# Optimization experiments

Hardware: AMD Instinct MI355X
Metric: run time of the kernel (lower is better)

The kernel has to match this reference:

```python
import jax, jax.numpy as jnp
import numpy as np
from jax.scipy.special import digamma, gammaln

COEF = 0.01
PRIOR = 1.0
IGNORE_INDEX = 255


def setup_inputs() -> dict:
    key = jax.random.key(0)
    k1, k2 = jax.random.split(key)
    pred = jax.random.normal(k1, (8, 19, 512, 512), dtype=jnp.float32)
    target = jax.random.randint(k2, (8, 512, 512), 0, 19, dtype=jnp.int64)
    return {"pred": pred, "target": target}


def reference(pred, target):
    # pred: [B, C, H, W] logits; target: [B, H, W] int class ids
    alphas = jnp.exp(pred)
    mask_ignore = target == IGNORE_INDEX
    tgt = jnp.where(mask_ignore, 0, target)
    # gather alpha at the answer class: [B, H, W]
    a_ans = jnp.take_along_axis(alphas, tgt[:, None, :, :], axis=1)[:, 0]
    a_zero = jnp.sum(alphas, axis=1)  # [B, H, W]
    ll_loss = digamma(a_ans) - digamma(a_zero)
    loss1 = gammaln(a_zero) - jnp.sum(gammaln(alphas), axis=1)
    loss2 = jnp.sum((alphas - PRIOR) * (digamma(alphas) - digamma(a_zero)[:, None, :, :]), axis=1)
    kl_loss = loss1 + loss2
    loss = COEF * kl_loss - ll_loss  # [B, H, W]
    loss = jnp.where(mask_ignore, jnp.zeros_like(loss), loss)
    avg_factor = jnp.sum(target != IGNORE_INDEX).astype(loss.dtype)
    return jnp.sum(loss) / avg_factor
```

## Files before the change

kernel.cpp:

```cpp
#include <hip/hip_runtime.h>


#define NCLS 19
#define HW (512 * 512)
#define NPIX (8 * HW)
#define IGNORE_IDX 255

#define PC1 0.08333333333f
#define PC2 0.00833333333f
#define PC3 0.00396825397f
#define GL1 0.08333333333f
#define GL2 0.00277777778f
#define GL3 0.00079365079f
#define HLN2PI 0.9189385332f
#define SUM_HLN2PI 17.45983213f

__device__ __forceinline__ float fast_rcp(float x) { return __builtin_amdgcn_rcpf(x); }

struct Acc {
    float a0, s2, slgy, sx, dgans;
};

__device__ __forceinline__ void chan(float x, int c, int tc, Acc& A) {
    float a   = __expf(x);
    float y   = a + 1.f;
    float rpy = fast_rcp(a * y);
    float r   = a * rpy;
    float rp  = y * rpy;
    float ly  = __logf(y);
    float r2  = r * r;
    float T   = __fmaf_rn(-r2, __fmaf_rn(-r2, PC3, PC2), PC1);
    float psiy = __fmaf_rn(-r2, T, __fmaf_rn(-0.5f, r, ly));
    float psia = psiy - rp;
    A.s2 = __fmaf_rn(a - 1.f, psia, A.s2);
    A.a0 += a;
    float G   = __fmaf_rn(-r2, __fmaf_rn(-r2, GL3, GL2), GL1);
    float lgp = __fmaf_rn(y - 0.5f, ly, -y);
    A.slgy = __fmaf_rn(r, G, A.slgy + lgp);
    A.sx += x;
    A.dgans = (c == tc) ? psia : A.dgans;
}

__device__ __forceinline__ float finish(const Acc& A) {
    float a0  = A.a0;
    float y   = a0 + 1.f;
    float rpy = fast_rcp(a0 * y);
    float r   = a0 * rpy;
    float rp  = y * rpy;
    float ly  = __logf(y);
    float la  = __logf(a0);
    float r2  = r * r;
    float T   = __fmaf_rn(-r2, __fmaf_rn(-r2, PC3, PC2), PC1);
    float psi0 = __fmaf_rn(-r2, T, __fmaf_rn(-0.5f, r, ly)) - rp;
    float G   = __fmaf_rn(-r2, __fmaf_rn(-r2, GL3, GL2), GL1);
    float lg0 = __fmaf_rn(y - 0.5f, ly, -y) + HLN2PI + r * G - la;

    float sum_lg = A.slgy + SUM_HLN2PI - A.sx;
    float ll    = A.dgans - psi0;
    float loss1 = lg0 - sum_lg;
    float loss2 = A.s2 - psi0 * (a0 - (float)NCLS);
    return 0.01f * (loss1 + loss2) - ll;
}

__global__ __launch_bounds__(256, 2) void bml_main(const float* __restrict__ pred,
                                                   const int* __restrict__ target,
                                                   double* __restrict__ ws) {
    int tid = blockIdx.x * blockDim.x + threadIdx.x;
    int p4  = tid << 2;
    int b   = p4 >> 18;
    int hw  = p4 & (HW - 1);
    const float4* base = (const float4*)(pred + (size_t)b * NCLS * HW + hw);

    int4 t4 = *(const int4*)(target + p4);
    int tc0 = (t4.x == IGNORE_IDX) ? 0 : t4.x;
    int tc1 = (t4.y == IGNORE_IDX) ? 0 : t4.y;
    int tc2 = (t4.z == IGNORE_IDX) ? 0 : t4.z;
    int tc3 = (t4.w == IGNORE_IDX) ? 0 : t4.w;

    float4 xs[NCLS];
    #pragma unroll
    for (int c = 0; c < NCLS; ++c)
        xs[c] = base[c * (HW / 4)];
    __builtin_amdgcn_sched_barrier(0);

    Acc A0 = {0.f, 0.f, 0.f, 0.f, 0.f};
    Acc A1 = {0.f, 0.f, 0.f, 0.f, 0.f};
    Acc A2 = {0.f, 0.f, 0.f, 0.f, 0.f};
    Acc A3 = {0.f, 0.f, 0.f, 0.f, 0.f};
    #pragma unroll
    for (int c = 0; c < NCLS; ++c) {
        chan(xs[c].x, c, tc0, A0);
        chan(xs[c].y, c, tc1, A1);
        chan(xs[c].z, c, tc2, A2);
        chan(xs[c].w, c, tc3, A3);
    }

    float l0 = finish(A0), l1 = finish(A1), l2 = finish(A2), l3 = finish(A3);

    float local = 0.f;
    unsigned cnt = 0;
    if (t4.x != IGNORE_IDX) { local += l0; cnt++; }
    if (t4.y != IGNORE_IDX) { local += l1; cnt++; }
    if (t4.z != IGNORE_IDX) { local += l2; cnt++; }
    if (t4.w != IGNORE_IDX) { local += l3; cnt++; }

    #pragma unroll
    for (int off = 32; off; off >>= 1) {
        local += __shfl_down(local, off);
        cnt   += __shfl_down(cnt, off);
    }
    __shared__ float s_sum[4];
    __shared__ unsigned s_cnt[4];
    int lane = threadIdx.x & 63, wid = threadIdx.x >> 6;
    if (lane == 0) { s_sum[wid] = local; s_cnt[wid] = cnt; }
    __syncthreads();
    if (threadIdx.x == 0) {
        float bs = s_sum[0] + s_sum[1] + s_sum[2] + s_sum[3];
        unsigned bc = s_cnt[0] + s_cnt[1] + s_cnt[2] + s_cnt[3];
        atomicAdd(&ws[0], (double)bs);
        atomicAdd(&ws[1], (double)bc);
    }
}

__global__ void bml_finalize(const double* __restrict__ ws, float* __restrict__ out) {
    if (threadIdx.x == 0 && blockIdx.x == 0)
        out[0] = (float)(ws[0] / ws[1]);
}

extern "C" void kernel_launch(void* const* d_in, const int* in_sizes, int n_in,
                              void* d_out, int out_size, void* d_ws, size_t ws_size,
                              hipStream_t stream) {
    const float* pred = (const float*)d_in[0];
    const int* target = (const int*)d_in[1];
    float* out = (float*)d_out;
    double* ws = (double*)d_ws;

    hipMemsetAsync(d_ws, 0, 2 * sizeof(double), stream);

    const int block = 256;
    const int grid = NPIX / (block * 4);
    bml_main<<<grid, block, 0, stream>>>(pred, target, ws);
    bml_finalize<<<1, 64, 0, stream>>>(ws, out);
}
```

Measured before the change: 244.3 us.

## Replace double atomics and memset with per-block partials and tree-reduced finalize

Each block now writes its partial sum and count to its own slot in the workspace, and a 256-thread finalize kernel reduces those slots in double precision. This removes the memset launch and the 4096 contended double atomicAdds. The change also folds the sum-of-x accumulator into the lgamma accumulator, moves the target load after the pred loads, and raises launch_bounds occupancy from 2 to 4 blocks per CU, which may force register spilling given 76 live float values per thread.

```diff
diff --git a/kernel.cpp b/kernel.cpp
--- a/kernel.cpp
+++ b/kernel.cpp
@@ -4,6 +4,7 @@
 #define NCLS 19
 #define HW (512 * 512)
 #define NPIX (8 * HW)
+#define NBLK 2048
 #define IGNORE_IDX 255
 
 #define PC1 0.08333333333f
@@ -18,7 +19,7 @@
 __device__ __forceinline__ float fast_rcp(float x) { return __builtin_amdgcn_rcpf(x); }
 
 struct Acc {
-    float a0, s2, slgy, sx, dgans;
+    float a0, s2, slgx, dgans;
 };
 
 __device__ __forceinline__ void chan(float x, int c, int tc, Acc& A) {
@@ -35,9 +36,8 @@
     A.s2 = __fmaf_rn(a - 1.f, psia, A.s2);
     A.a0 += a;
     float G   = __fmaf_rn(-r2, __fmaf_rn(-r2, GL3, GL2), GL1);
-    float lgp = __fmaf_rn(y - 0.5f, ly, -y);
-    A.slgy = __fmaf_rn(r, G, A.slgy + lgp);
-    A.sx += x;
+    float lgp = __fmaf_rn(y - 0.5f, ly, -y) - x;
+    A.slgx = __fmaf_rn(r, G, A.slgx + lgp);
     A.dgans = (c == tc) ? psia : A.dgans;
 }
 
@@ -55,38 +55,38 @@
     float G   = __fmaf_rn(-r2, __fmaf_rn(-r2, GL3, GL2), GL1);
     float lg0 = __fmaf_rn(y - 0.5f, ly, -y) + HLN2PI + r * G - la;
 
-    float sum_lg = A.slgy + SUM_HLN2PI - A.sx;
+    float sum_lg = A.slgx + SUM_HLN2PI;
     float ll    = A.dgans - psi0;
     float loss1 = lg0 - sum_lg;
     float loss2 = A.s2 - psi0 * (a0 - (float)NCLS);
     return 0.01f * (loss1 + loss2) - ll;
 }
 
-__global__ __launch_bounds__(256, 2) void bml_main(const float* __restrict__ pred,
+__global__ __launch_bounds__(256, 4) void bml_main(const float* __restrict__ pred,
                                                    const int* __restrict__ target,
-                                                   double* __restrict__ ws) {
+                                                   float* __restrict__ partial) {
     int tid = blockIdx.x * blockDim.x + threadIdx.x;
     int p4  = tid << 2;
     int b   = p4 >> 18;
     int hw  = p4 & (HW - 1);
     const float4* base = (const float4*)(pred + (size_t)b * NCLS * HW + hw);
 
+    float4 xs[NCLS];
+    #pragma unroll
+    for (int c = 0; c < NCLS; ++c)
+        xs[c] = base[c * (HW / 4)];
     int4 t4 = *(const int4*)(target + p4);
+    __builtin_amdgcn_sched_barrier(0);
+
     int tc0 = (t4.x == IGNORE_IDX) ? 0 : t4.x;
     int tc1 = (t4.y == IGNORE_IDX) ? 0 : t4.y;
     int tc2 = (t4.z == IGNORE_IDX) ? 0 : t4.z;
     int tc3 = (t4.w == IGNORE_IDX) ? 0 : t4.w;
 
-    float4 xs[NCLS];
-    #pragma unroll
-    for (int c = 0; c < NCLS; ++c)
-        xs[c] = base[c * (HW / 4)];
-    __builtin_amdgcn_sched_barrier(0);
-
-    Acc A0 = {0.f, 0.f, 0.f, 0.f, 0.f};
-    Acc A1 = {0.f, 0.f, 0.f, 0.f, 0.f};
-    Acc A2 = {0.f, 0.f, 0.f, 0.f, 0.f};
-    Acc A3 = {0.f, 0.f, 0.f, 0.f, 0.f};
+    Acc A0 = {0.f, 0.f, 0.f, 0.f};
+    Acc A1 = {0.f, 0.f, 0.f, 0.f};
+    Acc A2 = {0.f, 0.f, 0.f, 0.f};
+    Acc A3 = {0.f, 0.f, 0.f, 0.f};
     #pragma unroll
     for (int c = 0; c < NCLS; ++c) {
         chan(xs[c].x, c, tc0, A0);
@@ -98,11 +98,11 @@
     float l0 = finish(A0), l1 = finish(A1), l2 = finish(A2), l3 = finish(A3);
 
     float local = 0.f;
-    unsigned cnt = 0;
-    if (t4.x != IGNORE_IDX) { local += l0; cnt++; }
-    if (t4.y != IGNORE_IDX) { local += l1; cnt++; }
-    if (t4.z != IGNORE_IDX) { local += l2; cnt++; }
-    if (t4.w != IGNORE_IDX) { local += l3; cnt++; }
+    float cnt = 0.f;
+    if (t4.x != IGNORE_IDX) { local += l0; cnt += 1.f; }
+    if (t4.y != IGNORE_IDX) { local += l1; cnt += 1.f; }
+    if (t4.z != IGNORE_IDX) { local += l2; cnt += 1.f; }
+    if (t4.w != IGNORE_IDX) { local += l3; cnt += 1.f; }
 
     #pragma unroll
     for (int off = 32; off; off >>= 1) {
@@ -110,21 +110,37 @@
         cnt   += __shfl_down(cnt, off);
     }
     __shared__ float s_sum[4];
-    __shared__ unsigned s_cnt[4];
+    __shared__ float s_cnt[4];
     int lane = threadIdx.x & 63, wid = threadIdx.x >> 6;
     if (lane == 0) { s_sum[wid] = local; s_cnt[wid] = cnt; }
     __syncthreads();
     if (threadIdx.x == 0) {
-        float bs = s_sum[0] + s_sum[1] + s_sum[2] + s_sum[3];
-        unsigned bc = s_cnt[0] + s_cnt[1] + s_cnt[2] + s_cnt[3];
-        atomicAdd(&ws[0], (double)bs);
-        atomicAdd(&ws[1], (double)bc);
+        partial[blockIdx.x]        = s_sum[0] + s_sum[1] + s_sum[2] + s_sum[3];
+        partial[NBLK + blockIdx.x] = s_cnt[0] + s_cnt[1] + s_cnt[2] + s_cnt[3];
     }
 }
 
-__global__ void bml_finalize(const double* __restrict__ ws, float* __restrict__ out) {
-    if (threadIdx.x == 0 && blockIdx.x == 0)
-        out[0] = (float)(ws[0] / ws[1]);
+__global__ __launch_bounds__(256) void bml_finalize(const float* __restrict__ partial,
+                                                    float* __restrict__ out) {
+    double s = 0.0, n = 0.0;
+    for (int i = threadIdx.x; i < NBLK; i += 256) {
+        s += (double)partial[i];
+        n += (double)partial[NBLK + i];
+    }
+    #pragma unroll
+    for (int off = 32; off; off >>= 1) {
+        s += __shfl_down(s, off);
+        n += __shfl_down(n, off);
+    }
+    __shared__ double sh_s[4], sh_n[4];
+    int lane = threadIdx.x & 63, wid = threadIdx.x >> 6;
+    if (lane == 0) { sh_s[wid] = s; sh_n[wid] = n; }
+    __syncthreads();
+    if (threadIdx.x == 0) {
+        double ts = sh_s[0] + sh_s[1] + sh_s[2] + sh_s[3];
+        double tn = sh_n[0] + sh_n[1] + sh_n[2] + sh_n[3];
+        out[0] = (float)(ts / tn);
+    }
 }
 
 extern "C" void kernel_launch(void* const* d_in, const int* in_sizes, int n_in,
@@ -133,12 +149,9 @@
     const float* pred = (const float*)d_in[0];
     const int* target = (const int*)d_in[1];
     float* out = (float*)d_out;
-    double* ws = (double*)d_ws;
-
-    hipMemsetAsync(d_ws, 0, 2 * sizeof(double), stream);
+    float* partial = (float*)d_ws;
 
     const int block = 256;
-    const int grid = NPIX / (block * 4);
-    bml_main<<<grid, block, 0, stream>>>(pred, target, ws);
-    bml_finalize<<<1, 64, 0, stream>>>(ws, out);
+    bml_main<<<NBLK, block, 0, stream>>>(pred, target, partial);
+    bml_finalize<<<1, 256, 0, stream>>>(partial, out);
 }
```

Result: faster. 233.2 us (-4.5%).
